# Kernel tuning notes

Hardware: AMD Instinct MI355X
Metric: run time of the kernel (lower is better)

## Reference

```python
import jax, jax.numpy as jnp
import numpy as np

N, K, D, H = 2048, 128, 768, 512


def setup_inputs() -> dict:
    key = jax.random.key(0)
    k1, k2, k3, k4, k5, k6 = jax.random.split(key, 6)
    image_feat = jax.random.normal(k1, (N, D), dtype=jnp.float32)
    text_feat = jax.random.normal(k2, (K, D), dtype=jnp.float32)
    # nn.Linear(2D, H): weight (H, 2D), bias (H); stored transposed for clean matmul
    W1 = jax.random.normal(k3, (2 * D, H), dtype=jnp.float32) * (1.0 / np.sqrt(2 * D))
    b1 = jax.random.normal(k4, (H,), dtype=jnp.float32) * 0.01
    # nn.Linear(H, 1)
    W2 = jax.random.normal(k5, (H, 1), dtype=jnp.float32) * (1.0 / np.sqrt(H))
    b2 = jax.random.normal(k6, (1,), dtype=jnp.float32) * 0.01
    return {"image_feat": image_feat, "text_feat": text_feat,
            "W1": W1, "b1": b1, "W2": W2, "b2": b2}


def reference(image_feat, text_feat, W1, b1, W2, b2):
    # concat([img, txt]) @ W1 == img @ W1[:D] + txt @ W1[D:]  (same math,
    # avoids materializing the (N,K,2D) concatenated tensor)
    img_proj = image_feat @ W1[:D]          # (N, H)
    txt_proj = text_feat @ W1[D:]           # (K, H)
    h = jax.nn.relu(img_proj[:, None, :] + txt_proj[None, :, :] + b1)  # (N, K, H)
    sim = (h @ W2).squeeze(-1) + b2[0]      # (N, K)
    return sim
```

## Files before the change

### kernel.cpp

```cpp
#include <hip/hip_runtime.h>
#include <hip/hip_bf16.h>

#define N_IMG 2048
#define K_TXT 128
#define D_IN  768
#define H_DIM 512
#define M_TOT (N_IMG + K_TXT)
#define NK    (N_IMG * K_TXT)

typedef __bf16 bf16x8 __attribute__((ext_vector_type(8)));
typedef float  f32x4  __attribute__((ext_vector_type(4)));

__global__ __launch_bounds__(256) void proj_kernel(
    const float* __restrict__ img, const float* __restrict__ txt,
    const float* __restrict__ W1, const float* __restrict__ b1,
    float* __restrict__ P)
{
    __shared__ __align__(16) __bf16 As[2][64][32];
    __shared__ __align__(16) __bf16 Bs[2][64][32];

    const int tid = threadIdx.x;
    const int n0 = blockIdx.x * 64;
    const int m0 = blockIdx.y * 64;
    const bool is_txt = (m0 >= N_IMG);
    const float* X  = is_txt ? (txt + (size_t)(m0 - N_IMG) * D_IN)
                             : (img + (size_t)m0 * D_IN);
    const float* Wb = W1 + (is_txt ? (size_t)D_IN * H_DIM : 0);

    const int wave = tid >> 6, lane = tid & 63;
    const int wm = (wave >> 1) * 32, wn = (wave & 1) * 32;
    const int quad = lane >> 4, lm = lane & 15;

    const int ar  = tid >> 2, akq = tid & 3;
    const int bn  = tid & 63, bq  = tid >> 6;

    f32x4 acc[2][2] = {};

    f32x4 aR[4];
    float bR[16];

    auto loadA = [&](int kc) {
        const float* ap = X + (size_t)ar * D_IN + kc + akq * 16;
        aR[0] = *(const f32x4*)(ap + 0);
        aR[1] = *(const f32x4*)(ap + 4);
        aR[2] = *(const f32x4*)(ap + 8);
        aR[3] = *(const f32x4*)(ap + 12);
    };
    auto loadB = [&](int kc) {
        #pragma unroll
        for (int j2 = 0; j2 < 2; ++j2)
            #pragma unroll
            for (int j = 0; j < 8; ++j)
                bR[j2 * 8 + j] =
                    Wb[(size_t)(kc + j2 * 32 + bq * 8 + j) * H_DIM + n0 + bn];
    };

    union BPack { __bf16 h[8]; uint4 u; };

    loadA(0); loadB(0);

    for (int it = 0; it < 12; ++it) {
        {
            const int sub = akq >> 1, off = (akq & 1) * 16;
            BPack p0, p1;
            #pragma unroll
            for (int j = 0; j < 4; ++j) { p0.h[j] = (__bf16)aR[0][j]; p0.h[4+j] = (__bf16)aR[1][j]; }
            #pragma unroll
            for (int j = 0; j < 4; ++j) { p1.h[j] = (__bf16)aR[2][j]; p1.h[4+j] = (__bf16)aR[3][j]; }
            *(uint4*)&As[sub][ar][off]     = p0.u;
            *(uint4*)&As[sub][ar][off + 8] = p1.u;
            BPack q0, q1;
            #pragma unroll
            for (int j = 0; j < 8; ++j) { q0.h[j] = (__bf16)bR[j]; q1.h[j] = (__bf16)bR[8 + j]; }
            *(uint4*)&Bs[0][bn][bq * 8] = q0.u;
            *(uint4*)&Bs[1][bn][bq * 8] = q1.u;
        }
        __syncthreads();

        if (it < 11) { loadA((it + 1) * 64); loadB((it + 1) * 64); }

        #pragma unroll
        for (int sub = 0; sub < 2; ++sub) {
            bf16x8 af0 = *(bf16x8*)&As[sub][wm +  0 + lm][quad * 8];
            bf16x8 af1 = *(bf16x8*)&As[sub][wm + 16 + lm][quad * 8];
            bf16x8 bf0 = *(bf16x8*)&Bs[sub][wn +  0 + lm][quad * 8];
            bf16x8 bf1 = *(bf16x8*)&Bs[sub][wn + 16 + lm][quad * 8];
            acc[0][0] = __builtin_amdgcn_mfma_f32_16x16x32_bf16(af0, bf0, acc[0][0], 0, 0, 0);
            acc[0][1] = __builtin_amdgcn_mfma_f32_16x16x32_bf16(af0, bf1, acc[0][1], 0, 0, 0);
            acc[1][0] = __builtin_amdgcn_mfma_f32_16x16x32_bf16(af1, bf0, acc[1][0], 0, 0, 0);
            acc[1][1] = __builtin_amdgcn_mfma_f32_16x16x32_bf16(af1, bf1, acc[1][1], 0, 0, 0);
        }
        __syncthreads();
    }

    #pragma unroll
    for (int i = 0; i < 2; ++i) {
        #pragma unroll
        for (int j = 0; j < 2; ++j) {
            const int gn = n0 + wn + j * 16 + lm;
            const float badd = is_txt ? b1[gn] : 0.0f;
            #pragma unroll
            for (int r = 0; r < 4; ++r) {
                const int gm = m0 + wm + i * 16 + quad * 4 + r;
                P[(size_t)gm * H_DIM + gn] = acc[i][j][r] + badd;
            }
        }
    }
}

__global__ __launch_bounds__(256) void pw_kernel(
    const float* __restrict__ P, const float* __restrict__ W2,
    float* __restrict__ pw)
{
    const int row  = blockIdx.x * 4 + (threadIdx.x >> 6);
    const int lane = threadIdx.x & 63;
    const float* p = P + (size_t)row * H_DIM;
    float acc = 0.f;
    #pragma unroll
    for (int base = 0; base < H_DIM; base += 256) {
        f32x4 pv = *(const f32x4*)(p  + base + lane * 4);
        f32x4 wv = *(const f32x4*)(W2 + base + lane * 4);
        acc += pv[0]*wv[0] + pv[1]*wv[1] + pv[2]*wv[2] + pv[3]*wv[3];
    }
    #pragma unroll
    for (int off = 32; off > 0; off >>= 1) acc += __shfl_down(acc, off, 64);
    if (lane == 0) pw[row] = 0.5f * acc;
}

__global__ __launch_bounds__(256) void sim_kernel(
    const float* __restrict__ P, const float* __restrict__ W2,
    float* __restrict__ P2)
{
    __shared__ __align__(16) float Bs[64][67];
    __shared__ __align__(16) float Ws[64];

    const int tid = threadIdx.x;
    const int n0 = blockIdx.x * 32;
    const int k0 = blockIdx.y * 64;
    const int hs = blockIdx.z;
    const int hc = hs * 64;

    #pragma unroll
    for (int i = 0; i < 4; ++i) {
        const int flat = tid + i * 256;
        const int row = flat >> 4, c4 = flat & 15;
        f32x4 v = *(const f32x4*)(P + (size_t)(N_IMG + k0 + row) * H_DIM + hc + c4 * 4);
        *(f32x4*)&Bs[row][c4 * 4] = v;
    }
    if (tid < 16) {
        f32x4 w = *(const f32x4*)(W2 + hc + tid * 4);
        w *= 0.5f;
        *(f32x4*)&Ws[tid * 4] = w;
    }
    __syncthreads();

    const int tx = tid & 15;
    const int ty = tid >> 4;
    const float* pA = P + (size_t)(n0 + ty * 2) * H_DIM + hc;

    f32x4 acc0 = {0.f, 0.f, 0.f, 0.f};
    f32x4 acc1 = {0.f, 0.f, 0.f, 0.f};

    #pragma unroll 4
    for (int h4 = 0; h4 < 16; ++h4) {
        f32x4 a0 = *(const f32x4*)(pA + h4 * 4);
        f32x4 a1 = *(const f32x4*)(pA + H_DIM + h4 * 4);
        f32x4 w  = *(f32x4*)&Ws[h4 * 4];
        f32x4 b[4];
        #pragma unroll
        for (int j = 0; j < 4; ++j) b[j] = *(f32x4*)&Bs[tx * 4 + j][h4 * 4];

        #pragma unroll
        for (int j = 0; j < 4; ++j) {
            #pragma unroll
            for (int hh = 0; hh < 4; ++hh) {
                const float t0 = a0[hh] + b[j][hh];
                acc0[j] = fmaf(fabsf(t0), w[hh], acc0[j]);
                const float t1 = a1[hh] + b[j][hh];
                acc1[j] = fmaf(fabsf(t1), w[hh], acc1[j]);
            }
        }
    }

    float* o = P2 + (size_t)hs * NK + (size_t)(n0 + ty * 2) * K_TXT + k0 + tx * 4;
    *(f32x4*)o = acc0;
    *(f32x4*)(o + K_TXT) = acc1;
}

__global__ __launch_bounds__(256) void reduce_kernel(
    const float* __restrict__ P2, const float* __restrict__ pw,
    const float* __restrict__ b2, float* __restrict__ out)
{
    const int idx = blockIdx.x * 256 + threadIdx.x;
    const int n  = idx >> 5;
    const int k4 = (idx & 31) * 4;
    const size_t base = (size_t)n * K_TXT + k4;

    f32x4 s = {0.f, 0.f, 0.f, 0.f};
    #pragma unroll
    for (int hs = 0; hs < 8; ++hs)
        s += *(const f32x4*)(P2 + (size_t)hs * NK + base);

    const float add = pw[n] + b2[0];
    f32x4 pk = *(const f32x4*)(pw + N_IMG + k4);
    s[0] += add + pk[0]; s[1] += add + pk[1];
    s[2] += add + pk[2]; s[3] += add + pk[3];
    *(f32x4*)(out + base) = s;
}

extern "C" void kernel_launch(void* const* d_in, const int* in_sizes, int n_in,
                              void* d_out, int out_size, void* d_ws, size_t ws_size,
                              hipStream_t stream) {
    const float* img = (const float*)d_in[0];
    const float* txt = (const float*)d_in[1];
    const float* W1  = (const float*)d_in[2];
    const float* b1  = (const float*)d_in[3];
    const float* W2  = (const float*)d_in[4];
    const float* b2  = (const float*)d_in[5];
    float* out = (float*)d_out;

    float* P  = (float*)d_ws;
    float* pw = P + (size_t)M_TOT * H_DIM;
    float* P2 = pw + M_TOT;

    proj_kernel  <<<dim3(H_DIM / 64, M_TOT / 64), 256, 0, stream>>>(img, txt, W1, b1, P);
    pw_kernel    <<<dim3(M_TOT / 4),              256, 0, stream>>>(P, W2, pw);
    sim_kernel   <<<dim3(N_IMG / 32, K_TXT / 64, H_DIM / 64), 256, 0, stream>>>(P, W2, P2);
    reduce_kernel<<<dim3(NK / 4 / 256),           256, 0, stream>>>(P2, pw, b2, out);
}
```

Baseline: 105.7 us.

## Fuse W2 row-dot into projection epilogue and shrink proj tiles to 32x64

Removes the separate pw_kernel by computing each row's half-weighted dot with W2 in the projection epilogue, reducing across lanes with shuffles and accumulating with atomicAdd into a zeroed pw buffer. The projection tile is cut from 64x64 to 32x64 so the grid doubles to 544 blocks for better CU occupancy, and the LDS layout becomes a single padded 64-wide K tile. This trades one kernel launch and a reread of P for a memset, atomics, and a lower compute-to-load ratio per block.

```diff
diff --git a/kernel.cpp b/kernel.cpp
--- a/kernel.cpp
+++ b/kernel.cpp
@@ -14,45 +14,40 @@
 __global__ __launch_bounds__(256) void proj_kernel(
     const float* __restrict__ img, const float* __restrict__ txt,
     const float* __restrict__ W1, const float* __restrict__ b1,
-    float* __restrict__ P)
+    const float* __restrict__ W2, float* __restrict__ P,
+    float* __restrict__ pw)
 {
-    __shared__ __align__(16) __bf16 As[2][64][32];
-    __shared__ __align__(16) __bf16 Bs[2][64][32];
+    __shared__ __align__(16) __bf16 As[32][72];
+    __shared__ __align__(16) __bf16 Bs[64][72];
 
     const int tid = threadIdx.x;
-    const int n0 = blockIdx.x * 64;
-    const int m0 = blockIdx.y * 64;
+    const int n0 = (blockIdx.x & 7) * 64;
+    const int m0 = (blockIdx.x >> 3) * 32;
     const bool is_txt = (m0 >= N_IMG);
     const float* X  = is_txt ? (txt + (size_t)(m0 - N_IMG) * D_IN)
                              : (img + (size_t)m0 * D_IN);
     const float* Wb = W1 + (is_txt ? (size_t)D_IN * H_DIM : 0);
 
     const int wave = tid >> 6, lane = tid & 63;
-    const int wm = (wave >> 1) * 32, wn = (wave & 1) * 32;
+    const int wm = (wave >> 1) * 16, wn = (wave & 1) * 32;
     const int quad = lane >> 4, lm = lane & 15;
 
-    const int ar  = tid >> 2, akq = tid & 3;
-    const int bn  = tid & 63, bq  = tid >> 6;
-
-    f32x4 acc[2][2] = {};
-
-    f32x4 aR[4];
+    const int ar = tid >> 3, ak = (tid & 7) * 8;
+    const int bn = tid & 63, bk = (tid >> 6) * 16;
+
+    f32x4 acc[2] = {};
+    f32x4 aR0, aR1;
     float bR[16];
 
     auto loadA = [&](int kc) {
-        const float* ap = X + (size_t)ar * D_IN + kc + akq * 16;
-        aR[0] = *(const f32x4*)(ap + 0);
-        aR[1] = *(const f32x4*)(ap + 4);
-        aR[2] = *(const f32x4*)(ap + 8);
-        aR[3] = *(const f32x4*)(ap + 12);
+        const float* ap = X + (size_t)ar * D_IN + kc + ak;
+        aR0 = *(const f32x4*)(ap + 0);
+        aR1 = *(const f32x4*)(ap + 4);
     };
     auto loadB = [&](int kc) {
         #pragma unroll
-        for (int j2 = 0; j2 < 2; ++j2)
-            #pragma unroll
-            for (int j = 0; j < 8; ++j)
-                bR[j2 * 8 + j] =
-                    Wb[(size_t)(kc + j2 * 32 + bq * 8 + j) * H_DIM + n0 + bn];
+        for (int j = 0; j < 16; ++j)
+            bR[j] = Wb[(size_t)(kc + bk + j) * H_DIM + n0 + bn];
     };
 
     union BPack { __bf16 h[8]; uint4 u; };
@@ -60,71 +55,54 @@
     loadA(0); loadB(0);
 
     for (int it = 0; it < 12; ++it) {
-        {
-            const int sub = akq >> 1, off = (akq & 1) * 16;
-            BPack p0, p1;
-            #pragma unroll
-            for (int j = 0; j < 4; ++j) { p0.h[j] = (__bf16)aR[0][j]; p0.h[4+j] = (__bf16)aR[1][j]; }
-            #pragma unroll
-            for (int j = 0; j < 4; ++j) { p1.h[j] = (__bf16)aR[2][j]; p1.h[4+j] = (__bf16)aR[3][j]; }
-            *(uint4*)&As[sub][ar][off]     = p0.u;
-            *(uint4*)&As[sub][ar][off + 8] = p1.u;
-            BPack q0, q1;
-            #pragma unroll
-            for (int j = 0; j < 8; ++j) { q0.h[j] = (__bf16)bR[j]; q1.h[j] = (__bf16)bR[8 + j]; }
-            *(uint4*)&Bs[0][bn][bq * 8] = q0.u;
-            *(uint4*)&Bs[1][bn][bq * 8] = q1.u;
+        BPack pa;
+        #pragma unroll
+        for (int j = 0; j < 4; ++j) { pa.h[j] = (__bf16)aR0[j]; pa.h[4+j] = (__bf16)aR1[j]; }
+        *(uint4*)&As[ar][ak] = pa.u;
+        BPack q0, q1;
+        #pragma unroll
+        for (int j = 0; j < 8; ++j) { q0.h[j] = (__bf16)bR[j]; q1.h[j] = (__bf16)bR[8+j]; }
+        *(uint4*)&Bs[bn][bk]     = q0.u;
+        *(uint4*)&Bs[bn][bk + 8] = q1.u;
+        __syncthreads();
+
+        if (it < 11) { loadA((it + 1) * 64); loadB((it + 1) * 64); }
+
+        #pragma unroll
+        for (int sub = 0; sub < 2; ++sub) {
+            bf16x8 af  = *(bf16x8*)&As[wm + lm][sub * 32 + quad * 8];
+            bf16x8 bf0 = *(bf16x8*)&Bs[wn +  0 + lm][sub * 32 + quad * 8];
+            bf16x8 bf1 = *(bf16x8*)&Bs[wn + 16 + lm][sub * 32 + quad * 8];
+            acc[0] = __builtin_amdgcn_mfma_f32_16x16x32_bf16(af, bf0, acc[0], 0, 0, 0);
+            acc[1] = __builtin_amdgcn_mfma_f32_16x16x32_bf16(af, bf1, acc[1], 0, 0, 0);
         }
         __syncthreads();
-
-        if (it < 11) { loadA((it + 1) * 64); loadB((it + 1) * 64); }
-
-        #pragma unroll
-        for (int sub = 0; sub < 2; ++sub) {
-            bf16x8 af0 = *(bf16x8*)&As[sub][wm +  0 + lm][quad * 8];
-            bf16x8 af1 = *(bf16x8*)&As[sub][wm + 16 + lm][quad * 8];
-            bf16x8 bf0 = *(bf16x8*)&Bs[sub][wn +  0 + lm][quad * 8];
-            bf16x8 bf1 = *(bf16x8*)&Bs[sub][wn + 16 + lm][quad * 8];
-            acc[0][0] = __builtin_amdgcn_mfma_f32_16x16x32_bf16(af0, bf0, acc[0][0], 0, 0, 0);
-            acc[0][1] = __builtin_amdgcn_mfma_f32_16x16x32_bf16(af0, bf1, acc[0][1], 0, 0, 0);
-            acc[1][0] = __builtin_amdgcn_mfma_f32_16x16x32_bf16(af1, bf0, acc[1][0], 0, 0, 0);
-            acc[1][1] = __builtin_amdgcn_mfma_f32_16x16x32_bf16(af1, bf1, acc[1][1], 0, 0, 0);
+    }
+
+    float rv[4] = {0.f, 0.f, 0.f, 0.f};
+    #pragma unroll
+    for (int j = 0; j < 2; ++j) {
+        const int gn = n0 + wn + j * 16 + lm;
+        const float badd = is_txt ? b1[gn] : 0.0f;
+        const float w2h = 0.5f * W2[gn];
+        #pragma unroll
+        for (int r = 0; r < 4; ++r) {
+            const int gm = m0 + wm + quad * 4 + r;
+            const float v = acc[j][r] + badd;
+            P[(size_t)gm * H_DIM + gn] = v;
+            rv[r] = fmaf(v, w2h, rv[r]);
         }
-        __syncthreads();
-    }
-
-    #pragma unroll
-    for (int i = 0; i < 2; ++i) {
-        #pragma unroll
-        for (int j = 0; j < 2; ++j) {
-            const int gn = n0 + wn + j * 16 + lm;
-            const float badd = is_txt ? b1[gn] : 0.0f;
-            #pragma unroll
-            for (int r = 0; r < 4; ++r) {
-                const int gm = m0 + wm + i * 16 + quad * 4 + r;
-                P[(size_t)gm * H_DIM + gn] = acc[i][j][r] + badd;
-            }
-        }
-    }
-}
-
-__global__ __launch_bounds__(256) void pw_kernel(
-    const float* __restrict__ P, const float* __restrict__ W2,
-    float* __restrict__ pw)
-{
-    const int row  = blockIdx.x * 4 + (threadIdx.x >> 6);
-    const int lane = threadIdx.x & 63;
-    const float* p = P + (size_t)row * H_DIM;
-    float acc = 0.f;
-    #pragma unroll
-    for (int base = 0; base < H_DIM; base += 256) {
-        f32x4 pv = *(const f32x4*)(p  + base + lane * 4);
-        f32x4 wv = *(const f32x4*)(W2 + base + lane * 4);
-        acc += pv[0]*wv[0] + pv[1]*wv[1] + pv[2]*wv[2] + pv[3]*wv[3];
-    }
-    #pragma unroll
-    for (int off = 32; off > 0; off >>= 1) acc += __shfl_down(acc, off, 64);
-    if (lane == 0) pw[row] = 0.5f * acc;
+    }
+    #pragma unroll
+    for (int m = 1; m < 16; m <<= 1) {
+        #pragma unroll
+        for (int r = 0; r < 4; ++r) rv[r] += __shfl_xor(rv[r], m, 64);
+    }
+    if (lm == 0) {
+        #pragma unroll
+        for (int r = 0; r < 4; ++r)
+            atomicAdd(&pw[m0 + wm + quad * 4 + r], rv[r]);
+    }
 }
 
 __global__ __launch_bounds__(256) void sim_kernel(
@@ -223,8 +201,9 @@
     float* pw = P + (size_t)M_TOT * H_DIM;
     float* P2 = pw + M_TOT;
 
-    proj_kernel  <<<dim3(H_DIM / 64, M_TOT / 64), 256, 0, stream>>>(img, txt, W1, b1, P);
-    pw_kernel    <<<dim3(M_TOT / 4),              256, 0, stream>>>(P, W2, pw);
+    hipMemsetAsync(pw, 0, M_TOT * sizeof(float), stream);
+
+    proj_kernel  <<<dim3(544),                256, 0, stream>>>(img, txt, W1, b1, W2, P, pw);
     sim_kernel   <<<dim3(N_IMG / 32, K_TXT / 64, H_DIM / 64), 256, 0, stream>>>(P, W2, P2);
-    reduce_kernel<<<dim3(NK / 4 / 256),           256, 0, stream>>>(P2, pw, b2, out);
-}
+    reduce_kernel<<<dim3(NK / 4 / 256),       256, 0, stream>>>(P2, pw, b2, out);
+}
```

Result: faster. 101.7 us (-3.8%).
